# Kernel tuning notes

Measured on AMD Instinct MI355X. Metric: run time of the kernel, lower is better.

The kernel has to match this reference:

```python
import jax, jax.numpy as jnp
import numpy as np

K = 10  # kNN neighbors (module default)


def _safe_norm(x):
    # norm along last axis with zero (not NaN) gradient at x == 0
    sq = jnp.sum(x * x, axis=-1)
    safe = jnp.where(sq > 0, sq, 1.0)
    return jnp.where(sq > 0, jnp.sqrt(safe), 0.0)


def _angle(v1, v2):
    cross = jnp.cross(v1, v2, axis=-1)
    dot = jnp.sum(v1 * v2, axis=-1)
    return jnp.arctan2(_safe_norm(cross), dot)


def _compute_normals(p, k):
    # squared pairwise distances (same kNN ordering as cdist, cheaper/safer)
    sq = jnp.sum((p[:, None, :] - p[None, :, :]) ** 2, axis=-1)  # (N,N)
    _, knn = jax.lax.top_k(-sq, k + 1)
    knn = knn[:, 1:]                        # drop self, (N,k)
    neigh = p[knn]                          # (N,k,3)
    centered = neigh - neigh.mean(axis=1, keepdims=True)
    cov = jnp.einsum('nki,nkj->nij', centered, centered) / k  # (N,3,3)
    _, eigvecs = jnp.linalg.eigh(cov)
    return eigvecs[:, :, 0]                 # smallest-eigenvalue eigenvector, (N,3)


def reference(points, W, b):
    p = points[0]                           # (N,3)
    n = _compute_normals(p, K)              # (N,3)
    d = p[:, None, :] - p[None, :, :]       # (N,N,3), d[i,j] = p_i - p_j
    ni = jnp.broadcast_to(n[:, None, :], d.shape)
    nj = jnp.broadcast_to(n[None, :, :], d.shape)
    ppf = jnp.stack([
        _safe_norm(d),
        _angle(ni, d),
        _angle(nj, d),
        _angle(ni, nj),
    ], axis=-1)                             # (N,N,4)
    feat = ppf.mean(axis=1)                 # (N,4)
    s = feat @ W.T + b                      # (N,out)
    return s[None]                          # (1,N,out)


def setup_inputs() -> dict:
    key = jax.random.key(0)
    k1, k2 = jax.random.split(key)
    N, OUT = 2048, 256
    points = jax.random.normal(k1, (1, N, 3), dtype=jnp.float32)
    W = jax.random.normal(k2, (OUT, 4), dtype=jnp.float32) * 0.1
    b = jnp.zeros((OUT,), dtype=jnp.float32)
    return {"points": points, "W": W, "b": b}
```

## Files before the change

### kernel.cpp

```cpp
#include <hip/hip_runtime.h>
#include <math.h>

#pragma clang fp contract(off)

#define NPTS 2048
#define KNN 10
#define NOUT 256


__device__ __forceinline__ float lapy2f(float x, float y) {
  float xa = fabsf(x), ya = fabsf(y);
  float w = fmaxf(xa, ya), z = fminf(xa, ya);
  if (z == 0.f) return w;
  float t = z / w;
  return w * sqrtf(1.f + t * t);
}

__device__ __forceinline__ void slartgf(float f, float g, float& c, float& s, float& r) {
  if (g == 0.f) { c = 1.f; s = 0.f; r = f; }
  else if (f == 0.f) { c = 0.f; s = copysignf(1.f, g); r = fabsf(g); }
  else {
    float d = sqrtf(f * f + g * g);
    float p = 1.f / d;
    c = fabsf(f) * p;
    s = g * copysignf(p, f);
    r = copysignf(d, f);
  }
}

__device__ __forceinline__ void slaev2f(float a, float b, float c,
                                        float& rt1, float& rt2, float& cs1, float& sn1) {
  float sm = a + c;
  float df = a - c;
  float adf = fabsf(df);
  float tb = b + b;
  float ab = fabsf(tb);
  float acmx, acmn;
  if (fabsf(a) > fabsf(c)) { acmx = a; acmn = c; } else { acmx = c; acmn = a; }
  float rt;
  if (adf > ab)      { float t = ab / adf; rt = adf * sqrtf(1.f + t * t); }
  else if (adf < ab) { float t = adf / ab; rt = ab * sqrtf(1.f + t * t); }
  else               { rt = ab * sqrtf(2.f); }
  int sgn1;
  if (sm < 0.f) {
    rt1 = 0.5f * (sm - rt); sgn1 = -1;
    rt2 = (acmx / rt1) * acmn - (b / rt1) * b;
  } else if (sm > 0.f) {
    rt1 = 0.5f * (sm + rt); sgn1 = 1;
    rt2 = (acmx / rt1) * acmn - (b / rt1) * b;
  } else {
    rt1 = 0.5f * rt; rt2 = -0.5f * rt; sgn1 = 1;
  }
  int sgn2; float cs;
  if (df >= 0.f) { cs = df + rt; sgn2 = 1; } else { cs = df - rt; sgn2 = -1; }
  float acs = fabsf(cs);
  if (acs > ab) {
    float ct = -tb / cs;
    sn1 = 1.f / sqrtf(1.f + ct * ct);
    cs1 = ct * sn1;
  } else {
    if (ab == 0.f) { cs1 = 1.f; sn1 = 0.f; }
    else {
      float tn = -cs / tb;
      cs1 = 1.f / sqrtf(1.f + tn * tn);
      sn1 = tn * cs1;
    }
  }
  if (sgn1 == sgn2) { float tn = cs1; cs1 = -sn1; sn1 = tn; }
}

#define ROT12(c, s) {                                         \
    float t_;                                                 \
    t_ = z01; z01 = (c) * t_ - (s) * z00; z00 = (s) * t_ + (c) * z00; \
    t_ = z11; z11 = (c) * t_ - (s) * z10; z10 = (s) * t_ + (c) * z10; \
    t_ = z21; z21 = (c) * t_ - (s) * z20; z20 = (s) * t_ + (c) * z20; }
#define ROT23(c, s) {                                         \
    float t_;                                                 \
    t_ = z02; z02 = (c) * t_ - (s) * z01; z01 = (s) * t_ + (c) * z01; \
    t_ = z12; z12 = (c) * t_ - (s) * z11; z11 = (s) * t_ + (c) * z11; \
    t_ = z22; z22 = (c) * t_ - (s) * z21; z21 = (s) * t_ + (c) * z21; }

__device__ __forceinline__ void ssteqr3_reg(
    float& d0, float& d1, float& d2, float& e0, float& e1,
    float& z00, float& z01, float& z02,
    float& z10, float& z11, float& z12,
    float& z20, float& z21, float& z22) {
  const float eps = 5.9604645e-8f;
  const float eps2 = eps * eps;
  const float safmin = 1.1754944e-38f;
  const int nmaxit = 90;
  int jtot = 0;
  int l1 = 1;
  for (int og = 0; og < 4; ++og) {
    if (l1 > 3) break;
    if (l1 == 2) e0 = 0.f;
    else if (l1 == 3) e1 = 0.f;
    int m = 3;
    if (l1 == 1) {
      float t = fabsf(e0);
      if (t == 0.f) m = 1;
      else if (t <= (sqrtf(fabsf(d0)) * sqrtf(fabsf(d1))) * eps) { e0 = 0.f; m = 1; }
      else {
        float t2 = fabsf(e1);
        if (t2 == 0.f) m = 2;
        else if (t2 <= (sqrtf(fabsf(d1)) * sqrtf(fabsf(d2))) * eps) { e1 = 0.f; m = 2; }
      }
    } else if (l1 == 2) {
      float t = fabsf(e1);
      if (t == 0.f) m = 2;
      else if (t <= (sqrtf(fabsf(d1)) * sqrtf(fabsf(d2))) * eps) { e1 = 0.f; m = 2; }
    }
    int l = l1, lend = m;
    l1 = m + 1;
    if (lend == l) continue;
    {
      float dlend = (lend == 1) ? d0 : ((lend == 2) ? d1 : d2);
      float dl = (l == 1) ? d0 : ((l == 2) ? d1 : d2);
      if (fabsf(dlend) < fabsf(dl)) { int t = lend; lend = l; l = t; }
    }
    if (lend > l) {
      for (int it = 0; it < 128; ++it) {
        int m2 = lend;
        if (l != lend) {
          for (int mm = l; mm <= lend - 1; ++mm) {
            float em  = (mm == 1) ? e0 : e1;
            float dm1 = (mm == 1) ? d0 : d1;
            float dm  = (mm == 1) ? d1 : d2;
            float tst = em * em;
            if (tst <= (eps2 * fabsf(dm1)) * fabsf(dm) + safmin) { m2 = mm; break; }
          }
        }
        if (m2 < lend) { if (m2 == 1) e0 = 0.f; else e1 = 0.f; }
        float p = (l == 1) ? d0 : ((l == 2) ? d1 : d2);
        if (m2 == l) { l += 1; if (l <= lend) continue; break; }
        if (m2 == l + 1) {
          float rt1, rt2, c, s;
          if (l == 1) {
            slaev2f(d0, e0, d1, rt1, rt2, c, s);
            ROT12(c, s)
            d0 = rt1; d1 = rt2; e0 = 0.f;
          } else {
            slaev2f(d1, e1, d2, rt1, rt2, c, s);
            ROT23(c, s)
            d1 = rt1; d2 = rt2; e1 = 0.f;
          }
          l += 2; if (l <= lend) continue; break;
        }
        if (jtot == nmaxit) break;
        jtot++;
        float g = (d1 - p) / (2.f * e0);
        float r = lapy2f(g, 1.f);
        g = d2 - p + e0 / (g + copysignf(r, g));
        float s = 1.f, c = 1.f;
        p = 0.f;
        float c0, s0n, c1, s1n;
        {
          float f = s * e1;
          float bb = c * e1;
          slartgf(g, f, c, s, r);
          g = d2 - p;
          r = (d1 - g) * s + 2.f * c * bb;
          p = s * r;
          d2 = g + p;
          g = c * r - bb;
          c1 = c; s1n = -s;
        }
        {
          float f = s * e0;
          float bb = c * e0;
          slartgf(g, f, c, s, r);
          e1 = r;
          g = d1 - p;
          r = (d0 - g) * s + 2.f * c * bb;
          p = s * r;
          d1 = g + p;
          g = c * r - bb;
          c0 = c; s0n = -s;
        }
        ROT23(c1, s1n)
        ROT12(c0, s0n)
        d0 = d0 - p;
        e0 = g;
      }
    } else {
      for (int it = 0; it < 128; ++it) {
        int m2 = lend;
        if (l != lend) {
          for (int mm = l; mm >= lend + 1; --mm) {
            float em  = (mm == 3) ? e1 : e0;
            float dm1 = (mm == 3) ? d2 : d1;
            float dm2 = (mm == 3) ? d1 : d0;
            float tst = em * em;
            if (tst <= (eps2 * fabsf(dm1)) * fabsf(dm2) + safmin) { m2 = mm; break; }
          }
        }
        if (m2 > lend) { if (m2 == 3) e1 = 0.f; else e0 = 0.f; }
        float p = (l == 1) ? d0 : ((l == 2) ? d1 : d2);
        if (m2 == l) { l -= 1; if (l >= lend) continue; break; }
        if (m2 == l - 1) {
          float rt1, rt2, c, s;
          if (l == 2) {
            slaev2f(d0, e0, d1, rt1, rt2, c, s);
            ROT12(c, s)
            d0 = rt1; d1 = rt2; e0 = 0.f;
          } else {
            slaev2f(d1, e1, d2, rt1, rt2, c, s);
            ROT23(c, s)
            d1 = rt1; d2 = rt2; e1 = 0.f;
          }
          l -= 2; if (l >= lend) continue; break;
        }
        if (jtot == nmaxit) break;
        jtot++;
        float g = (d1 - p) / (2.f * e1);
        float r = lapy2f(g, 1.f);
        g = d0 - p + e1 / (g + copysignf(r, g));
        float s = 1.f, c = 1.f;
        p = 0.f;
        float c0, s0p, c1, s1p;
        {
          float f = s * e0;
          float bb = c * e0;
          slartgf(g, f, c, s, r);
          g = d0 - p;
          r = (d1 - g) * s + 2.f * c * bb;
          p = s * r;
          d0 = g + p;
          g = c * r - bb;
          c0 = c; s0p = s;
        }
        {
          float f = s * e1;
          float bb = c * e1;
          slartgf(g, f, c, s, r);
          e0 = r;
          g = d1 - p;
          r = (d2 - g) * s + 2.f * c * bb;
          p = s * r;
          d1 = g + p;
          g = c * r - bb;
          c1 = c; s1p = s;
        }
        ROT12(c0, s0p)
        ROT23(c1, s1p)
        d2 = d2 - p;
        e1 = g;
      }
    }
  }
  {
    int k = 1; float p = d0;
    if (d1 < p) { k = 2; p = d1; }
    if (d2 < p) { k = 3; p = d2; }
    if (k == 2) {
      d1 = d0; d0 = p;
      float t;
      t = z00; z00 = z01; z01 = t;
      t = z10; z10 = z11; z11 = t;
      t = z20; z20 = z21; z21 = t;
    } else if (k == 3) {
      d2 = d0; d0 = p;
      float t;
      t = z00; z00 = z02; z02 = t;
      t = z10; z10 = z12; z12 = t;
      t = z20; z20 = z22; z22 = t;
    }
    k = 2; p = d1;
    if (d2 < p) { k = 3; p = d2; }
    if (k == 3) {
      d2 = d1; d1 = p;
      float t;
      t = z01; z01 = z02; z02 = t;
      t = z11; z11 = z12; z12 = t;
      t = z21; z21 = z22; z22 = t;
    }
  }
}


__global__ __launch_bounds__(64) void knn_select_kernel(const float* __restrict__ pts,
                                                        int* __restrict__ knn) {
  const int i = blockIdx.x;
  const int lane = threadIdx.x;
  float px = pts[3 * i], py = pts[3 * i + 1], pz = pts[3 * i + 2];

  unsigned long long k0[8], k1[8], k2[8], k3[8];
#define DIST(g, arr)                                                      \
  {                                                                       \
    _Pragma("unroll")                                                     \
    for (int t = 0; t < 8; ++t) {                                         \
      int j = ((g) * 8 + t) * 64 + lane;                                  \
      float dx = px - pts[3 * j];                                         \
      float dy = py - pts[3 * j + 1];                                     \
      float dz = pz - pts[3 * j + 2];                                     \
      float sq = dx * dx;                                                 \
      sq = sq + dy * dy;                                                  \
      sq = sq + dz * dz;                                                  \
      arr[t] = (((unsigned long long)__float_as_uint(sq)) << 32) |        \
               (unsigned int)j;                                           \
    }                                                                     \
  }
  DIST(0, k0) DIST(1, k1) DIST(2, k2) DIST(3, k3)
#undef DIST

#define CE(arr, a, b)                                                     \
  {                                                                       \
    unsigned long long lo = arr[a] < arr[b] ? arr[a] : arr[b];            \
    unsigned long long hi = arr[a] < arr[b] ? arr[b] : arr[a];            \
    arr[a] = lo; arr[b] = hi;                                             \
  }
#define SORT8(arr)                                                        \
  CE(arr, 0, 1) CE(arr, 2, 3) CE(arr, 4, 5) CE(arr, 6, 7)                 \
  CE(arr, 0, 2) CE(arr, 1, 3) CE(arr, 4, 6) CE(arr, 5, 7)                 \
  CE(arr, 1, 2) CE(arr, 5, 6) CE(arr, 0, 4) CE(arr, 3, 7)                 \
  CE(arr, 1, 5) CE(arr, 2, 6)                                             \
  CE(arr, 1, 4) CE(arr, 3, 6)                                             \
  CE(arr, 2, 4) CE(arr, 3, 5)                                             \
  CE(arr, 3, 4)
  SORT8(k0) SORT8(k1) SORT8(k2) SORT8(k3)
#undef SORT8
#undef CE

#define POP(arr)                                                          \
  {                                                                       \
    _Pragma("unroll")                                                     \
    for (int q = 0; q < 7; ++q) arr[q] = arr[q + 1];                      \
    arr[7] = 0xFFFFFFFFFFFFFFFFULL;                                       \
  }

  for (int r = 0; r < KNN + 1; ++r) {
    unsigned long long h01 = k0[0] < k1[0] ? k0[0] : k1[0];
    unsigned long long h23 = k2[0] < k3[0] ? k2[0] : k3[0];
    unsigned long long h = h01 < h23 ? h01 : h23;
    unsigned long long m = h;
#pragma unroll
    for (int off = 32; off > 0; off >>= 1) {
      unsigned long long o = __shfl_xor(m, off, 64);
      m = (o < m) ? o : m;
    }
    if (r > 0 && lane == 0) knn[i * KNN + (r - 1)] = (int)(unsigned int)m;
    if (h == m) {
      if (k0[0] == m)      { POP(k0) }
      else if (k1[0] == m) { POP(k1) }
      else if (k2[0] == m) { POP(k2) }
      else                 { POP(k3) }
    }
  }
#undef POP
}


__global__ __launch_bounds__(64) void normals_kernel(const float* __restrict__ pts,
                                                     const int* __restrict__ knn,
                                                     float* __restrict__ nrm) {
  int i = blockIdx.x * 64 + threadIdx.x;

  float nx[KNN], ny[KNN], nz[KNN];
  float sx = 0.f, sy = 0.f, sz = 0.f;
#pragma unroll
  for (int t = 0; t < KNN; ++t) {
    int j = knn[i * KNN + t];
    nx[t] = pts[3 * j]; ny[t] = pts[3 * j + 1]; nz[t] = pts[3 * j + 2];
    sx = sx + nx[t]; sy = sy + ny[t]; sz = sz + nz[t];
  }
  float mx = sx / 10.f, my = sy / 10.f, mz = sz / 10.f;
  float a11 = 0.f, a21 = 0.f, a31 = 0.f, a22 = 0.f, a32 = 0.f, a33 = 0.f;
#pragma unroll
  for (int t = 0; t < KNN; ++t) {
    float cx = nx[t] - mx, cy = ny[t] - my, cz = nz[t] - mz;
    a11 = a11 + cx * cx;
    a21 = a21 + cy * cx;
    a31 = a31 + cz * cx;
    a22 = a22 + cy * cy;
    a32 = a32 + cz * cy;
    a33 = a33 + cz * cz;
  }
  a11 = a11 / 10.f; a21 = a21 / 10.f; a31 = a31 / 10.f;
  a22 = a22 / 10.f; a32 = a32 / 10.f; a33 = a33 / 10.f;

  float d0, d1, d2, e0, e1, tau1 = 0.f, v2 = 0.f;
  {
    float alpha = a21;
    float xnorm = fabsf(a31);
    if (xnorm == 0.f) {
      tau1 = 0.f; v2 = 0.f;
      d0 = a11; d1 = a22; d2 = a33; e0 = alpha; e1 = a32;
    } else {
      float beta = -copysignf(lapy2f(alpha, xnorm), alpha);
      tau1 = (beta - alpha) / beta;
      v2 = a31 * (1.f / (alpha - beta));
      float y1 = tau1 * a22; y1 = y1 + tau1 * (a32 * v2);
      float y2 = tau1 * a32; y2 = y2 + (tau1 * v2) * a33;
      float dotv = y1; dotv = dotv + y2 * v2;
      float ac = -0.5f * tau1 * dotv;
      y1 = y1 + ac;
      y2 = y2 + ac * v2;
      float t1 = -y1, t2 = -1.f;
      a22 = (a22 + t1) + y1 * t2;
      a32 = (a32 + v2 * t1) + y2 * t2;
      float t1b = -y2, t2b = -v2;
      a33 = (a33 + v2 * t1b) + y2 * t2b;
      d0 = a11; d1 = a22; d2 = a33; e0 = beta; e1 = a32;
    }
  }
  float z00 = 1.f, z01 = 0.f, z02 = 0.f;
  float z10 = 0.f, z11 = 1.f, z12 = 0.f;
  float z20 = 0.f, z21 = 0.f, z22 = 1.f;
  ssteqr3_reg(d0, d1, d2, e0, e1,
              z00, z01, z02, z10, z11, z12, z20, z21, z22);
  if (tau1 != 0.f) {
    float w = tau1 * (z10 + v2 * z20);
    z10 = z10 - w;
    z20 = z20 - v2 * w;
  }
  nrm[3 * i]     = z00;
  nrm[3 * i + 1] = z10;
  nrm[3 * i + 2] = z20;
}


__device__ __forceinline__ float atan2_pos(float y, float x) {
#pragma clang fp contract(fast)
  float axx = fabsf(x);
  float mn = fminf(axx, y), mx = fmaxf(axx, y);
  float a = mn * __builtin_amdgcn_rcpf(mx);
  a = (mx == 0.f) ? 0.f : a;
  float s = a * a;
  float r = a * (0.9998660f +
           s * (-0.3302995f +
           s * (0.1801410f +
           s * (-0.0851330f +
           s * 0.0208351f))));
  r = (y > axx) ? 1.57079632679f - r : r;
  r = (x < 0.f) ? 3.14159265359f - r : r;
  return r;
}

__device__ __forceinline__ float angle3(float ax, float ay, float az,
                                        float bx, float by, float bz) {
#pragma clang fp contract(fast)
  float cx = ay * bz - az * by;
  float cy = az * bx - ax * bz;
  float cz = ax * by - ay * bx;
  float sq = cx * cx + cy * cy + cz * cz;
  float dot = ax * bx + ay * by + az * bz;
  return atan2_pos(sqrtf(sq), dot);
}

__global__ __launch_bounds__(256) void ppf_kernel(const float* __restrict__ pts,
                                                  const float* __restrict__ nrm,
                                                  const float* __restrict__ Wm,
                                                  const float* __restrict__ bias,
                                                  float* __restrict__ out) {
#pragma clang fp contract(fast)
  int i = blockIdx.x;
  float px = pts[3 * i], py = pts[3 * i + 1], pz = pts[3 * i + 2];
  float ax = nrm[3 * i], ay = nrm[3 * i + 1], az = nrm[3 * i + 2];
  float s0 = 0.f, s1 = 0.f, s2 = 0.f, s3 = 0.f;
  for (int j = threadIdx.x; j < NPTS; j += 256) {
    float dx = px - pts[3 * j];
    float dy = py - pts[3 * j + 1];
    float dz = pz - pts[3 * j + 2];
    float bx = nrm[3 * j], by = nrm[3 * j + 1], bz = nrm[3 * j + 2];
    float sq = dx * dx + dy * dy + dz * dz;
    s0 += sqrtf(sq);
    s1 += angle3(ax, ay, az, dx, dy, dz);
    s2 += angle3(bx, by, bz, dx, dy, dz);
    s3 += angle3(ax, ay, az, bx, by, bz);
  }
  __shared__ float red[4][256];
  int tid = threadIdx.x;
  red[0][tid] = s0; red[1][tid] = s1; red[2][tid] = s2; red[3][tid] = s3;
  __syncthreads();
  for (int off = 128; off > 0; off >>= 1) {
    if (tid < off) {
      red[0][tid] += red[0][tid + off];
      red[1][tid] += red[1][tid + off];
      red[2][tid] += red[2][tid + off];
      red[3][tid] += red[3][tid + off];
    }
    __syncthreads();
  }
  float f0 = red[0][0] / 2048.f;
  float f1 = red[1][0] / 2048.f;
  float f2 = red[2][0] / 2048.f;
  float f3 = red[3][0] / 2048.f;
  int o = tid;
  float w0 = Wm[4 * o], w1 = Wm[4 * o + 1], w2 = Wm[4 * o + 2], w3 = Wm[4 * o + 3];
  out[i * NOUT + o] = (((f0 * w0 + f1 * w1) + f2 * w2) + f3 * w3) + bias[o];
}


extern "C" void kernel_launch(void* const* d_in, const int* in_sizes, int n_in,
                              void* d_out, int out_size, void* d_ws, size_t ws_size,
                              hipStream_t stream) {
  const float* pts = (const float*)d_in[0];
  const float* Wm  = (const float*)d_in[1];
  const float* bs  = (const float*)d_in[2];
  float* out = (float*)d_out;
  float* nrm = (float*)d_ws;
  int*   knn = (int*)((char*)d_ws + NPTS * 3 * sizeof(float));

  knn_select_kernel<<<NPTS, 64, 0, stream>>>(pts, knn);
  normals_kernel<<<NPTS / 64, 64, 0, stream>>>(pts, knn, nrm);
  ppf_kernel<<<NPTS, 256, 0, stream>>>(pts, nrm, Wm, bs, out);
}
```

Before: 109.1 us.

## Fuse kNN and normals kernels, use SoA layout and wave-per-point PPF

Merges the kNN selection and normal estimation into one kernel, with four wavefronts per block and the neighbor indices kept in LDS, which removes one launch and the global round trip for the indices. Points and normals are written in structure-of-arrays form so the PPF loop makes coalesced loads. The PPF kernel now gives each point one wavefront, replacing the LDS tree reduction and barriers with shuffles, and writes its output with float4 stores. The risk is that normals are now computed by only 4 threads per block, which serialises that step inside each block.

```diff
diff --git a/kernel.cpp b/kernel.cpp
--- a/kernel.cpp
+++ b/kernel.cpp
@@ -278,144 +278,149 @@
 }
 
 
-__global__ __launch_bounds__(64) void knn_select_kernel(const float* __restrict__ pts,
-                                                        int* __restrict__ knn) {
-  const int i = blockIdx.x;
-  const int lane = threadIdx.x;
-  float px = pts[3 * i], py = pts[3 * i + 1], pz = pts[3 * i + 2];
-
-  unsigned long long k0[8], k1[8], k2[8], k3[8];
+__global__ __launch_bounds__(256) void knn_normals_kernel(
+    const float* __restrict__ pts,
+    float* __restrict__ pxa, float* __restrict__ pya, float* __restrict__ pza,
+    float* __restrict__ nxa, float* __restrict__ nya, float* __restrict__ nza) {
+  __shared__ int knn_lds[4][KNN];
+  const int tid = threadIdx.x;
+  const int lane = tid & 63;
+  const int wv = tid >> 6;
+
+  {
+    const int p = 4 * blockIdx.x + wv;
+    float px = pts[3 * p], py = pts[3 * p + 1], pz = pts[3 * p + 2];
+    if (lane == 0) { pxa[p] = px; pya[p] = py; pza[p] = pz; }
+
+    unsigned long long k0[8], k1[8], k2[8], k3[8];
 #define DIST(g, arr)                                                      \
-  {                                                                       \
-    _Pragma("unroll")                                                     \
-    for (int t = 0; t < 8; ++t) {                                         \
-      int j = ((g) * 8 + t) * 64 + lane;                                  \
-      float dx = px - pts[3 * j];                                         \
-      float dy = py - pts[3 * j + 1];                                     \
-      float dz = pz - pts[3 * j + 2];                                     \
-      float sq = dx * dx;                                                 \
-      sq = sq + dy * dy;                                                  \
-      sq = sq + dz * dz;                                                  \
-      arr[t] = (((unsigned long long)__float_as_uint(sq)) << 32) |        \
-               (unsigned int)j;                                           \
-    }                                                                     \
-  }
-  DIST(0, k0) DIST(1, k1) DIST(2, k2) DIST(3, k3)
+    {                                                                     \
+      _Pragma("unroll")                                                   \
+      for (int t = 0; t < 8; ++t) {                                       \
+        int j = ((g) * 8 + t) * 64 + lane;                                \
+        float dx = px - pts[3 * j];                                       \
+        float dy = py - pts[3 * j + 1];                                   \
+        float dz = pz - pts[3 * j + 2];                                   \
+        float sq = dx * dx;                                               \
+        sq = sq + dy * dy;                                                \
+        sq = sq + dz * dz;                                                \
+        arr[t] = (((unsigned long long)__float_as_uint(sq)) << 32) |      \
+                 (unsigned int)j;                                         \
+      }                                                                   \
+    }
+    DIST(0, k0) DIST(1, k1) DIST(2, k2) DIST(3, k3)
 #undef DIST
 
 #define CE(arr, a, b)                                                     \
-  {                                                                       \
-    unsigned long long lo = arr[a] < arr[b] ? arr[a] : arr[b];            \
-    unsigned long long hi = arr[a] < arr[b] ? arr[b] : arr[a];            \
-    arr[a] = lo; arr[b] = hi;                                             \
-  }
+    {                                                                     \
+      unsigned long long lo = arr[a] < arr[b] ? arr[a] : arr[b];          \
+      unsigned long long hi = arr[a] < arr[b] ? arr[b] : arr[a];          \
+      arr[a] = lo; arr[b] = hi;                                           \
+    }
 #define SORT8(arr)                                                        \
-  CE(arr, 0, 1) CE(arr, 2, 3) CE(arr, 4, 5) CE(arr, 6, 7)                 \
-  CE(arr, 0, 2) CE(arr, 1, 3) CE(arr, 4, 6) CE(arr, 5, 7)                 \
-  CE(arr, 1, 2) CE(arr, 5, 6) CE(arr, 0, 4) CE(arr, 3, 7)                 \
-  CE(arr, 1, 5) CE(arr, 2, 6)                                             \
-  CE(arr, 1, 4) CE(arr, 3, 6)                                             \
-  CE(arr, 2, 4) CE(arr, 3, 5)                                             \
-  CE(arr, 3, 4)
-  SORT8(k0) SORT8(k1) SORT8(k2) SORT8(k3)
+    CE(arr, 0, 1) CE(arr, 2, 3) CE(arr, 4, 5) CE(arr, 6, 7)               \
+    CE(arr, 0, 2) CE(arr, 1, 3) CE(arr, 4, 6) CE(arr, 5, 7)               \
+    CE(arr, 1, 2) CE(arr, 5, 6) CE(arr, 0, 4) CE(arr, 3, 7)               \
+    CE(arr, 1, 5) CE(arr, 2, 6)                                           \
+    CE(arr, 1, 4) CE(arr, 3, 6)                                           \
+    CE(arr, 2, 4) CE(arr, 3, 5)                                           \
+    CE(arr, 3, 4)
+    SORT8(k0) SORT8(k1) SORT8(k2) SORT8(k3)
 #undef SORT8
 #undef CE
 
 #define POP(arr)                                                          \
-  {                                                                       \
-    _Pragma("unroll")                                                     \
-    for (int q = 0; q < 7; ++q) arr[q] = arr[q + 1];                      \
-    arr[7] = 0xFFFFFFFFFFFFFFFFULL;                                       \
-  }
-
-  for (int r = 0; r < KNN + 1; ++r) {
-    unsigned long long h01 = k0[0] < k1[0] ? k0[0] : k1[0];
-    unsigned long long h23 = k2[0] < k3[0] ? k2[0] : k3[0];
-    unsigned long long h = h01 < h23 ? h01 : h23;
-    unsigned long long m = h;
+    {                                                                     \
+      _Pragma("unroll")                                                   \
+      for (int q = 0; q < 7; ++q) arr[q] = arr[q + 1];                    \
+      arr[7] = 0xFFFFFFFFFFFFFFFFULL;                                     \
+    }
+    for (int r = 0; r < KNN + 1; ++r) {
+      unsigned long long h01 = k0[0] < k1[0] ? k0[0] : k1[0];
+      unsigned long long h23 = k2[0] < k3[0] ? k2[0] : k3[0];
+      unsigned long long h = h01 < h23 ? h01 : h23;
+      unsigned long long m = h;
 #pragma unroll
-    for (int off = 32; off > 0; off >>= 1) {
-      unsigned long long o = __shfl_xor(m, off, 64);
-      m = (o < m) ? o : m;
-    }
-    if (r > 0 && lane == 0) knn[i * KNN + (r - 1)] = (int)(unsigned int)m;
-    if (h == m) {
-      if (k0[0] == m)      { POP(k0) }
-      else if (k1[0] == m) { POP(k1) }
-      else if (k2[0] == m) { POP(k2) }
-      else                 { POP(k3) }
-    }
-  }
+      for (int off = 32; off > 0; off >>= 1) {
+        unsigned long long o = __shfl_xor(m, off, 64);
+        m = (o < m) ? o : m;
+      }
+      if (r > 0 && lane == 0) knn_lds[wv][r - 1] = (int)(unsigned int)m;
+      if (h == m) {
+        if (k0[0] == m)      { POP(k0) }
+        else if (k1[0] == m) { POP(k1) }
+        else if (k2[0] == m) { POP(k2) }
+        else                 { POP(k3) }
+      }
+    }
 #undef POP
-}
-
-
-__global__ __launch_bounds__(64) void normals_kernel(const float* __restrict__ pts,
-                                                     const int* __restrict__ knn,
-                                                     float* __restrict__ nrm) {
-  int i = blockIdx.x * 64 + threadIdx.x;
-
-  float nx[KNN], ny[KNN], nz[KNN];
-  float sx = 0.f, sy = 0.f, sz = 0.f;
+  }
+  __syncthreads();
+
+  if (tid < 4) {
+    const int p = 4 * blockIdx.x + tid;
+    float nx[KNN], ny[KNN], nz[KNN];
+    float sx = 0.f, sy = 0.f, sz = 0.f;
 #pragma unroll
-  for (int t = 0; t < KNN; ++t) {
-    int j = knn[i * KNN + t];
-    nx[t] = pts[3 * j]; ny[t] = pts[3 * j + 1]; nz[t] = pts[3 * j + 2];
-    sx = sx + nx[t]; sy = sy + ny[t]; sz = sz + nz[t];
-  }
-  float mx = sx / 10.f, my = sy / 10.f, mz = sz / 10.f;
-  float a11 = 0.f, a21 = 0.f, a31 = 0.f, a22 = 0.f, a32 = 0.f, a33 = 0.f;
+    for (int t = 0; t < KNN; ++t) {
+      int j = knn_lds[tid][t];
+      nx[t] = pts[3 * j]; ny[t] = pts[3 * j + 1]; nz[t] = pts[3 * j + 2];
+      sx = sx + nx[t]; sy = sy + ny[t]; sz = sz + nz[t];
+    }
+    float mx = sx / 10.f, my = sy / 10.f, mz = sz / 10.f;
+    float a11 = 0.f, a21 = 0.f, a31 = 0.f, a22 = 0.f, a32 = 0.f, a33 = 0.f;
 #pragma unroll
-  for (int t = 0; t < KNN; ++t) {
-    float cx = nx[t] - mx, cy = ny[t] - my, cz = nz[t] - mz;
-    a11 = a11 + cx * cx;
-    a21 = a21 + cy * cx;
-    a31 = a31 + cz * cx;
-    a22 = a22 + cy * cy;
-    a32 = a32 + cz * cy;
-    a33 = a33 + cz * cz;
-  }
-  a11 = a11 / 10.f; a21 = a21 / 10.f; a31 = a31 / 10.f;
-  a22 = a22 / 10.f; a32 = a32 / 10.f; a33 = a33 / 10.f;
-
-  float d0, d1, d2, e0, e1, tau1 = 0.f, v2 = 0.f;
-  {
-    float alpha = a21;
-    float xnorm = fabsf(a31);
-    if (xnorm == 0.f) {
-      tau1 = 0.f; v2 = 0.f;
-      d0 = a11; d1 = a22; d2 = a33; e0 = alpha; e1 = a32;
-    } else {
-      float beta = -copysignf(lapy2f(alpha, xnorm), alpha);
-      tau1 = (beta - alpha) / beta;
-      v2 = a31 * (1.f / (alpha - beta));
-      float y1 = tau1 * a22; y1 = y1 + tau1 * (a32 * v2);
-      float y2 = tau1 * a32; y2 = y2 + (tau1 * v2) * a33;
-      float dotv = y1; dotv = dotv + y2 * v2;
-      float ac = -0.5f * tau1 * dotv;
-      y1 = y1 + ac;
-      y2 = y2 + ac * v2;
-      float t1 = -y1, t2 = -1.f;
-      a22 = (a22 + t1) + y1 * t2;
-      a32 = (a32 + v2 * t1) + y2 * t2;
-      float t1b = -y2, t2b = -v2;
-      a33 = (a33 + v2 * t1b) + y2 * t2b;
-      d0 = a11; d1 = a22; d2 = a33; e0 = beta; e1 = a32;
-    }
-  }
-  float z00 = 1.f, z01 = 0.f, z02 = 0.f;
-  float z10 = 0.f, z11 = 1.f, z12 = 0.f;
-  float z20 = 0.f, z21 = 0.f, z22 = 1.f;
-  ssteqr3_reg(d0, d1, d2, e0, e1,
-              z00, z01, z02, z10, z11, z12, z20, z21, z22);
-  if (tau1 != 0.f) {
-    float w = tau1 * (z10 + v2 * z20);
-    z10 = z10 - w;
-    z20 = z20 - v2 * w;
-  }
-  nrm[3 * i]     = z00;
-  nrm[3 * i + 1] = z10;
-  nrm[3 * i + 2] = z20;
+    for (int t = 0; t < KNN; ++t) {
+      float cx = nx[t] - mx, cy = ny[t] - my, cz = nz[t] - mz;
+      a11 = a11 + cx * cx;
+      a21 = a21 + cy * cx;
+      a31 = a31 + cz * cx;
+      a22 = a22 + cy * cy;
+      a32 = a32 + cz * cy;
+      a33 = a33 + cz * cz;
+    }
+    a11 = a11 / 10.f; a21 = a21 / 10.f; a31 = a31 / 10.f;
+    a22 = a22 / 10.f; a32 = a32 / 10.f; a33 = a33 / 10.f;
+
+    float d0, d1, d2, e0, e1, tau1 = 0.f, v2 = 0.f;
+    {
+      float alpha = a21;
+      float xnorm = fabsf(a31);
+      if (xnorm == 0.f) {
+        tau1 = 0.f; v2 = 0.f;
+        d0 = a11; d1 = a22; d2 = a33; e0 = alpha; e1 = a32;
+      } else {
+        float beta = -copysignf(lapy2f(alpha, xnorm), alpha);
+        tau1 = (beta - alpha) / beta;
+        v2 = a31 * (1.f / (alpha - beta));
+        float y1 = tau1 * a22; y1 = y1 + tau1 * (a32 * v2);
+        float y2 = tau1 * a32; y2 = y2 + (tau1 * v2) * a33;
+        float dotv = y1; dotv = dotv + y2 * v2;
+        float ac = -0.5f * tau1 * dotv;
+        y1 = y1 + ac;
+        y2 = y2 + ac * v2;
+        float t1 = -y1, t2 = -1.f;
+        a22 = (a22 + t1) + y1 * t2;
+        a32 = (a32 + v2 * t1) + y2 * t2;
+        float t1b = -y2, t2b = -v2;
+        a33 = (a33 + v2 * t1b) + y2 * t2b;
+        d0 = a11; d1 = a22; d2 = a33; e0 = beta; e1 = a32;
+      }
+    }
+    float z00 = 1.f, z01 = 0.f, z02 = 0.f;
+    float z10 = 0.f, z11 = 1.f, z12 = 0.f;
+    float z20 = 0.f, z21 = 0.f, z22 = 1.f;
+    ssteqr3_reg(d0, d1, d2, e0, e1,
+                z00, z01, z02, z10, z11, z12, z20, z21, z22);
+    if (tau1 != 0.f) {
+      float w = tau1 * (z10 + v2 * z20);
+      z10 = z10 - w;
+      z20 = z20 - v2 * w;
+    }
+    nxa[p] = z00;
+    nya[p] = z10;
+    nza[p] = z20;
+  }
 }
 
 
@@ -447,47 +452,59 @@
   return atan2_pos(sqrtf(sq), dot);
 }
 
-__global__ __launch_bounds__(256) void ppf_kernel(const float* __restrict__ pts,
-                                                  const float* __restrict__ nrm,
-                                                  const float* __restrict__ Wm,
-                                                  const float* __restrict__ bias,
-                                                  float* __restrict__ out) {
+__global__ __launch_bounds__(256) void ppf_kernel(
+    const float* __restrict__ pxa, const float* __restrict__ pya,
+    const float* __restrict__ pza, const float* __restrict__ nxa,
+    const float* __restrict__ nya, const float* __restrict__ nza,
+    const float* __restrict__ Wm, const float* __restrict__ bias,
+    float* __restrict__ out) {
 #pragma clang fp contract(fast)
-  int i = blockIdx.x;
-  float px = pts[3 * i], py = pts[3 * i + 1], pz = pts[3 * i + 2];
-  float ax = nrm[3 * i], ay = nrm[3 * i + 1], az = nrm[3 * i + 2];
+  const int tid = threadIdx.x;
+  const int lane = tid & 63;
+  const int wv = tid >> 6;
+  const int i = 4 * blockIdx.x + wv;
+
+  float pxi = pxa[i], pyi = pya[i], pzi = pza[i];
+  float ax = nxa[i], ay = nya[i], az = nza[i];
+
   float s0 = 0.f, s1 = 0.f, s2 = 0.f, s3 = 0.f;
-  for (int j = threadIdx.x; j < NPTS; j += 256) {
-    float dx = px - pts[3 * j];
-    float dy = py - pts[3 * j + 1];
-    float dz = pz - pts[3 * j + 2];
-    float bx = nrm[3 * j], by = nrm[3 * j + 1], bz = nrm[3 * j + 2];
+#pragma unroll 4
+  for (int it = 0; it < NPTS / 64; ++it) {
+    int j = it * 64 + lane;
+    float dx = pxi - pxa[j];
+    float dy = pyi - pya[j];
+    float dz = pzi - pza[j];
+    float bx = nxa[j], by = nya[j], bz = nza[j];
     float sq = dx * dx + dy * dy + dz * dz;
     s0 += sqrtf(sq);
     s1 += angle3(ax, ay, az, dx, dy, dz);
     s2 += angle3(bx, by, bz, dx, dy, dz);
     s3 += angle3(ax, ay, az, bx, by, bz);
   }
-  __shared__ float red[4][256];
-  int tid = threadIdx.x;
-  red[0][tid] = s0; red[1][tid] = s1; red[2][tid] = s2; red[3][tid] = s3;
-  __syncthreads();
-  for (int off = 128; off > 0; off >>= 1) {
-    if (tid < off) {
-      red[0][tid] += red[0][tid + off];
-      red[1][tid] += red[1][tid + off];
-      red[2][tid] += red[2][tid + off];
-      red[3][tid] += red[3][tid + off];
-    }
-    __syncthreads();
-  }
-  float f0 = red[0][0] / 2048.f;
-  float f1 = red[1][0] / 2048.f;
-  float f2 = red[2][0] / 2048.f;
-  float f3 = red[3][0] / 2048.f;
-  int o = tid;
-  float w0 = Wm[4 * o], w1 = Wm[4 * o + 1], w2 = Wm[4 * o + 2], w3 = Wm[4 * o + 3];
-  out[i * NOUT + o] = (((f0 * w0 + f1 * w1) + f2 * w2) + f3 * w3) + bias[o];
+
+#pragma unroll
+  for (int off = 1; off < 64; off <<= 1) {
+    s0 += __shfl_xor(s0, off, 64);
+    s1 += __shfl_xor(s1, off, 64);
+    s2 += __shfl_xor(s2, off, 64);
+    s3 += __shfl_xor(s3, off, 64);
+  }
+  const float inv = 1.f / 2048.f;
+  float f0 = s0 * inv, f1 = s1 * inv, f2 = s2 * inv, f3 = s3 * inv;
+
+  const float4* W4 = (const float4*)Wm;
+  const float4* b4 = (const float4*)bias;
+  float4 bb = b4[lane];
+  float4 w0 = W4[4 * lane + 0];
+  float4 w1 = W4[4 * lane + 1];
+  float4 w2 = W4[4 * lane + 2];
+  float4 w3 = W4[4 * lane + 3];
+  float4 r;
+  r.x = (((f0 * w0.x + f1 * w0.y) + f2 * w0.z) + f3 * w0.w) + bb.x;
+  r.y = (((f0 * w1.x + f1 * w1.y) + f2 * w1.z) + f3 * w1.w) + bb.y;
+  r.z = (((f0 * w2.x + f1 * w2.y) + f2 * w2.z) + f3 * w2.w) + bb.z;
+  r.w = (((f0 * w3.x + f1 * w3.y) + f2 * w3.z) + f3 * w3.w) + bb.w;
+  ((float4*)(out + (size_t)i * NOUT))[lane] = r;
 }
 
 
@@ -498,10 +515,14 @@
   const float* Wm  = (const float*)d_in[1];
   const float* bs  = (const float*)d_in[2];
   float* out = (float*)d_out;
-  float* nrm = (float*)d_ws;
-  int*   knn = (int*)((char*)d_ws + NPTS * 3 * sizeof(float));
-
-  knn_select_kernel<<<NPTS, 64, 0, stream>>>(pts, knn);
-  normals_kernel<<<NPTS / 64, 64, 0, stream>>>(pts, knn, nrm);
-  ppf_kernel<<<NPTS, 256, 0, stream>>>(pts, nrm, Wm, bs, out);
-}
+
+  float* pxa = (float*)d_ws;
+  float* pya = pxa + NPTS;
+  float* pza = pya + NPTS;
+  float* nxa = pza + NPTS;
+  float* nya = nxa + NPTS;
+  float* nza = nya + NPTS;
+
+  knn_normals_kernel<<<NPTS / 4, 256, 0, stream>>>(pts, pxa, pya, pza, nxa, nya, nza);
+  ppf_kernel<<<NPTS / 4, 256, 0, stream>>>(pxa, pya, pza, nxa, nya, nza, Wm, bs, out);
+}
```

New measurement: 108.4 us. No clear change (-0.6%).
